# Kernel optimization log

Measured on AMD Instinct MI355X. Metric: run time of the kernel, lower is better.

Reference implementation:

```python
import jax, jax.numpy as jnp
import numpy as np

NUM_HEADS = 12
SAMPLING_RATIO = 0.5


def setup_inputs() -> dict:
    key = jax.random.key(0)
    k1, k2, k3, k4 = jax.random.split(key, 4)
    B, N, C = 4, 2048, 768
    x = jax.random.normal(k1, (B, N, C), dtype=jnp.float32)
    # nn.Linear(dim, 3*dim, bias=False): weight [3C, C]; we store transposed [C, 3C]
    w_qkv = jax.random.normal(k2, (C, 3 * C), dtype=jnp.float32) * (1.0 / np.sqrt(C))
    w_proj = jax.random.normal(k3, (C, C), dtype=jnp.float32) * (1.0 / np.sqrt(C))
    b_proj = jax.random.normal(k4, (C,), dtype=jnp.float32) * 0.01
    return {"x": x, "w_qkv": w_qkv, "w_proj": w_proj, "b_proj": b_proj}


def reference(x, w_qkv, w_proj, b_proj):
    B, N, C = x.shape
    H = NUM_HEADS
    hd = C // H
    scale = hd ** (-0.5)
    keep_num = int(N * SAMPLING_RATIO)

    qkv = (x @ w_qkv).reshape(B, N, 3, H, hd).transpose(2, 0, 3, 1, 4)  # [3,B,H,N,hd]
    q, k, v = qkv[0], qkv[1], qkv[2]

    # query-norm based token selection per (B, H)
    scores = jnp.linalg.norm(q, axis=-1)                     # [B,H,N]
    _, keep_idx = jax.lax.top_k(scores, keep_num)            # [B,H,keep]
    idx = keep_idx[..., None]                                # [B,H,keep,1]
    k_sel = jnp.take_along_axis(k, idx, axis=2)              # [B,H,keep,hd]
    v_sel = jnp.take_along_axis(v, idx, axis=2)              # [B,H,keep,hd]

    attn = jnp.einsum("bhnd,bhkd->bhnk", q, k_sel) * scale   # [B,H,N,keep]
    attn = jax.nn.softmax(jnp.clip(attn, -50.0, 50.0), axis=-1)
    out = jnp.einsum("bhnk,bhkd->bhnd", attn, v_sel)         # [B,H,N,hd]
    out = out.transpose(0, 2, 1, 3).reshape(B, N, C)
    return jnp.clip(out @ w_proj + b_proj, -10.0, 10.0)
```

## Files before the change

kernel.cpp:

```cpp
#include <hip/hip_runtime.h>
#include <hip/hip_bf16.h>
#include <math.h>


#define B_  4
#define N_  2048
#define C_  768
#define H_  12
#define HD_ 64
#define KEEP_ 1024
#define BH_ (B_ * H_)
#define GK  768

typedef __attribute__((ext_vector_type(8))) short short8v;
typedef __attribute__((ext_vector_type(4))) float f32x4;
typedef __attribute__((ext_vector_type(8))) _Float16 f16x8;
typedef __attribute__((ext_vector_type(4))) _Float16 f16x4;

__device__ inline unsigned short f2bf(float f) {
    unsigned u = __float_as_uint(f);
    unsigned r = (u + 0x7fffu + ((u >> 16) & 1u)) >> 16;
    return (unsigned short)r;
}
__device__ inline float bf2f(unsigned short h) {
    return __uint_as_float(((unsigned)h) << 16);
}

__device__ inline void gload16(const void* g, void* l) {
    __builtin_amdgcn_global_load_lds(
        (const __attribute__((address_space(1))) unsigned int*)(g),
        (__attribute__((address_space(3))) unsigned int*)(l), 16, 0, 0);
}

__global__ __launch_bounds__(256) void split4_kernel(
    const float* __restrict__ in, _Float16* __restrict__ hi,
    _Float16* __restrict__ lo, int n4)
{
    int i = blockIdx.x * 256 + threadIdx.x;
    if (i >= n4) return;
    float4 v = reinterpret_cast<const float4*>(in)[i];
    f16x4 h, l;
    h[0] = (_Float16)v.x; l[0] = (_Float16)(v.x - (float)h[0]);
    h[1] = (_Float16)v.y; l[1] = (_Float16)(v.y - (float)h[1]);
    h[2] = (_Float16)v.z; l[2] = (_Float16)(v.z - (float)h[2]);
    h[3] = (_Float16)v.w; l[3] = (_Float16)(v.w - (float)h[3]);
    reinterpret_cast<f16x4*>(hi)[i] = h;
    reinterpret_cast<f16x4*>(lo)[i] = l;
}

__global__ __launch_bounds__(256) void tsplit_kernel(
    const float* __restrict__ W, _Float16* __restrict__ Th,
    _Float16* __restrict__ Tl, int N)
{
    __shared__ float t[32][33];
    int n0 = blockIdx.x * 32, k0 = blockIdx.y * 32;
    int r = threadIdx.x >> 3, c4 = (threadIdx.x & 7) << 2;
    float4 v = *reinterpret_cast<const float4*>(&W[(size_t)(k0 + r) * N + n0 + c4]);
    t[r][c4 + 0] = v.x; t[r][c4 + 1] = v.y; t[r][c4 + 2] = v.z; t[r][c4 + 3] = v.w;
    __syncthreads();
#pragma unroll
    for (int j = 0; j < 4; ++j) {
        float val = t[c4 + j][r];
        _Float16 h = (_Float16)val;
        size_t o = (size_t)(n0 + r) * GK + k0 + c4 + j;
        Th[o] = h;
        Tl[o] = (_Float16)(val - (float)h);
    }
}

template <bool EPI>
__global__ __launch_bounds__(256, 2) void mfma_gemm(
    const _Float16* __restrict__ Ah, const _Float16* __restrict__ Al,
    const _Float16* __restrict__ Bh, const _Float16* __restrict__ Bl,
    float* __restrict__ C, int N, const float* __restrict__ bias,
    int gx, int cpx)
{
    __shared__ _Float16 lds[4][128 * 64];

    const int sb = ((int)blockIdx.x & 7) * cpx + ((int)blockIdx.x >> 3);
    const int bx = sb % gx, by = sb / gx;
    const int row0 = by * 128, col0 = bx * 128;

    const int tid = threadIdx.x;
    const int wave = tid >> 6, lane = tid & 63;
    const int fr = lane & 15, grp = lane >> 4;
    const int wr = wave >> 1, wc = wave & 1;

    const int dr = lane >> 3, ch = lane & 7;
    const int sc = (ch ^ dr) * 8;

    const _Float16* srcs[4] = {
        Ah + (size_t)row0 * GK, Al + (size_t)row0 * GK,
        Bh + (size_t)col0 * GK, Bl + (size_t)col0 * GK };

    f32x4 acc[4][4];
#pragma unroll
    for (int mt = 0; mt < 4; ++mt)
#pragma unroll
        for (int nt = 0; nt < 4; ++nt) acc[mt][nt] = (f32x4)0.f;

    const int swz0 = ((0 + grp) ^ (fr & 7)) * 16;
    const int swz1 = ((4 + grp) ^ (fr & 7)) * 16;

    for (int k0 = 0; k0 < GK; k0 += 64) {
        __syncthreads();
#pragma unroll
        for (int t = 0; t < 4; ++t) {
            const _Float16* gsrc = srcs[t] + k0 + sc;
#pragma unroll
            for (int i = 0; i < 4; ++i) {
                int rb = wave * 32 + i * 8;
                gload16(gsrc + (size_t)(rb + dr) * GK, &lds[t][rb * 64]);
            }
        }
        __syncthreads();

        f16x8 fa[4][2][2];
#pragma unroll
        for (int mt = 0; mt < 4; ++mt) {
            int rbyte = (wr * 64 + mt * 16 + fr) * 128;
            fa[mt][0][0] = *(const f16x8*)((const char*)lds[0] + rbyte + swz0);
            fa[mt][1][0] = *(const f16x8*)((const char*)lds[0] + rbyte + swz1);
            fa[mt][0][1] = *(const f16x8*)((const char*)lds[1] + rbyte + swz0);
            fa[mt][1][1] = *(const f16x8*)((const char*)lds[1] + rbyte + swz1);
        }
#pragma unroll
        for (int nt = 0; nt < 4; ++nt) {
            int rbyte = (wc * 64 + nt * 16 + fr) * 128;
            f16x8 bh0 = *(const f16x8*)((const char*)lds[2] + rbyte + swz0);
            f16x8 bh1 = *(const f16x8*)((const char*)lds[2] + rbyte + swz1);
            f16x8 bl0 = *(const f16x8*)((const char*)lds[3] + rbyte + swz0);
            f16x8 bl1 = *(const f16x8*)((const char*)lds[3] + rbyte + swz1);
#pragma unroll
            for (int mt = 0; mt < 4; ++mt) {
                acc[mt][nt] = __builtin_amdgcn_mfma_f32_16x16x32_f16(fa[mt][0][0], bh0, acc[mt][nt], 0, 0, 0);
                acc[mt][nt] = __builtin_amdgcn_mfma_f32_16x16x32_f16(fa[mt][0][0], bl0, acc[mt][nt], 0, 0, 0);
                acc[mt][nt] = __builtin_amdgcn_mfma_f32_16x16x32_f16(fa[mt][0][1], bh0, acc[mt][nt], 0, 0, 0);
                acc[mt][nt] = __builtin_amdgcn_mfma_f32_16x16x32_f16(fa[mt][1][0], bh1, acc[mt][nt], 0, 0, 0);
                acc[mt][nt] = __builtin_amdgcn_mfma_f32_16x16x32_f16(fa[mt][1][0], bl1, acc[mt][nt], 0, 0, 0);
                acc[mt][nt] = __builtin_amdgcn_mfma_f32_16x16x32_f16(fa[mt][1][1], bh1, acc[mt][nt], 0, 0, 0);
            }
        }
    }

#pragma unroll
    for (int mt = 0; mt < 4; ++mt)
#pragma unroll
        for (int nt = 0; nt < 4; ++nt) {
            int col = col0 + wc * 64 + nt * 16 + fr;
            float bv = 0.f;
            if (EPI) bv = bias[col];
#pragma unroll
            for (int r = 0; r < 4; ++r) {
                int row = row0 + wr * 64 + mt * 16 + grp * 4 + r;
                float v = acc[mt][nt][r];
                if (EPI) v = fminf(fmaxf(v + bv, -10.f), 10.f);
                C[(size_t)row * N + col] = v;
            }
        }
}

__global__ __launch_bounds__(256) void score_kernel(
    const float* __restrict__ qkv, float* __restrict__ scores,
    _Float16* __restrict__ q_h)
{
    int w = blockIdx.x * 4 + (threadIdx.x >> 6);
    int lane = threadIdx.x & 63;
    int bh = w >> 11;
    int n = w & (N_ - 1);
    int b = bh / H_, h = bh % H_;
    float q = qkv[((size_t)b * N_ + n) * (3 * C_) + (size_t)h * HD_ + lane];
    q_h[((size_t)bh * N_ + n) * HD_ + lane] = (_Float16)q;
    float ss = q * q;
#pragma unroll
    for (int off = 32; off; off >>= 1) ss += __shfl_xor(ss, off);
    if (lane == 0) scores[(size_t)bh * N_ + n] = ss;
}

__global__ __launch_bounds__(1024) void topk_kernel(
    const float* __restrict__ scores, int* __restrict__ keepidx)
{
    __shared__ unsigned long long keys[N_];
    const int bh = blockIdx.x;
    const int tid = threadIdx.x;
    const float* sc = scores + (size_t)bh * N_;
    for (int i = tid; i < N_; i += 1024) {
        unsigned fb = __float_as_uint(sc[i]);
        keys[i] = ((unsigned long long)fb << 32) | (unsigned)(N_ - 1 - i);
    }
    __syncthreads();
    for (int k = 2; k <= N_; k <<= 1) {
        for (int j = k >> 1; j > 0; j >>= 1) {
            for (int i = tid; i < N_; i += 1024) {
                int ixj = i ^ j;
                if (ixj > i) {
                    unsigned long long a = keys[i], b = keys[ixj];
                    bool desc = ((i & k) == 0);
                    if (desc ? (a < b) : (a > b)) { keys[i] = b; keys[ixj] = a; }
                }
            }
            __syncthreads();
        }
    }
    if (tid < KEEP_) {
        keepidx[(size_t)bh * KEEP_ + tid] = (N_ - 1) - (int)(keys[tid] & 0xffffffffu);
    }
}

__global__ __launch_bounds__(256) void gather_kernel(
    const float* __restrict__ qkv, const int* __restrict__ keepidx,
    _Float16* __restrict__ k_h, _Float16* __restrict__ k_l,
    unsigned short* __restrict__ vT_h, unsigned short* __restrict__ vT_l)
{
    __shared__ float vS[64][65];
    const int bh = blockIdx.x >> 4;
    const int chunk = blockIdx.x & 15;
    const int b = bh / H_, h = bh % H_;
    const int wave = threadIdx.x >> 6, lane = threadIdx.x & 63;
    const int j0 = chunk * 64;

#pragma unroll
    for (int jj = 0; jj < 16; ++jj) {
        int j = wave * 16 + jj;
        int n = keepidx[(size_t)bh * KEEP_ + j0 + j];
        size_t base = ((size_t)b * N_ + n) * (3 * C_) + (size_t)h * HD_ + lane;
        float kv = qkv[base + C_];
        float vv = qkv[base + 2 * C_];
        _Float16 kh = (_Float16)kv;
        size_t ko = ((size_t)bh * KEEP_ + j0 + j) * HD_ + lane;
        k_h[ko] = kh;
        k_l[ko] = (_Float16)(kv - (float)kh);
        vS[j][lane] = vv;
    }
    __syncthreads();
#pragma unroll
    for (int dd = 0; dd < 16; ++dd) {
        int d = wave * 16 + dd;
        float vv = vS[lane][d];
        unsigned short vh = f2bf(vv);
        size_t vo = ((size_t)bh * HD_ + d) * KEEP_ + j0 + lane;
        vT_h[vo] = vh;
        vT_l[vo] = f2bf(vv - bf2f(vh));
    }
}

__global__ __launch_bounds__(256, 2) void attn_kernel(
    const _Float16* __restrict__ q_h,
    const _Float16* __restrict__ k_h, const _Float16* __restrict__ k_l,
    const unsigned short* __restrict__ vT_h, const unsigned short* __restrict__ vT_l,
    _Float16* __restrict__ aoh, _Float16* __restrict__ aol)
{
    int bid = ((int)blockIdx.x & 7) * 96 + ((int)blockIdx.x >> 3);
    const int bh = bid >> 4;
    const int qt = bid & 15;
    const int b = bh / H_, h = bh - b * H_;
    const int wave = threadIdx.x >> 6;
    const int lane = threadIdx.x & 63;
    const int row16 = lane & 15;
    const int grp = lane >> 4;

    __shared__ unsigned short sKV[4][64 * 64];
    __shared__ unsigned short pH[4][32][72];

    const int n0 = qt * 128 + wave * 32;

    f16x8 aQ[2][2];
#pragma unroll
    for (int mt = 0; mt < 2; ++mt)
#pragma unroll
        for (int ks = 0; ks < 2; ++ks)
            aQ[mt][ks] = *reinterpret_cast<const f16x8*>(
                q_h + ((size_t)bh * N_ + n0 + mt * 16 + row16) * HD_ + ks * 32 + grp * 8);

    const int dr = lane >> 3, ch = lane & 7;
    const int sc8 = (ch ^ dr) * 8;
    const unsigned short* gbase;
    int rs, ts;
    if (wave == 0)      { gbase = (const unsigned short*)k_h + (size_t)bh * KEEP_ * HD_; rs = 64;   ts = 64 * HD_; }
    else if (wave == 1) { gbase = (const unsigned short*)k_l + (size_t)bh * KEEP_ * HD_; rs = 64;   ts = 64 * HD_; }
    else if (wave == 2) { gbase = vT_h + (size_t)bh * HD_ * KEEP_;                        rs = KEEP_; ts = 64; }
    else                { gbase = vT_l + (size_t)bh * HD_ * KEEP_;                        rs = KEEP_; ts = 64; }
    unsigned short* ldst = sKV[wave];

    f32x4 o[2][4];
    float ps[2][4];
#pragma unroll
    for (int mt = 0; mt < 2; ++mt)
#pragma unroll
        for (int nt = 0; nt < 4; ++nt) o[mt][nt] = (f32x4)0.f;
#pragma unroll
    for (int mt = 0; mt < 2; ++mt)
#pragma unroll
        for (int r = 0; r < 4; ++r) ps[mt][r] = 1e-30f;

    const int swzA = ((0 + grp) ^ (row16 & 7)) * 8;
    const int swzB = ((4 + grp) ^ (row16 & 7)) * 8;

    for (int t = 0; t < KEEP_ / 64; ++t) {
        __syncthreads();
#pragma unroll
        for (int i = 0; i < 8; ++i)
            gload16(gbase + (size_t)(i * 8 + dr) * rs + t * ts + sc8, ldst + i * 512);
        __syncthreads();

        f32x4 sv[2][4];
#pragma unroll
        for (int mt = 0; mt < 2; ++mt)
#pragma unroll
            for (int nt = 0; nt < 4; ++nt) sv[mt][nt] = (f32x4)0.f;
        const _Float16* sKh = (const _Float16*)sKV[0];
        const _Float16* sKl = (const _Float16*)sKV[1];
#pragma unroll
        for (int nt = 0; nt < 4; ++nt) {
            int rb = (nt * 16 + row16) * 64;
            f16x8 kh0 = *(const f16x8*)(sKh + rb + swzA);
            f16x8 kh1 = *(const f16x8*)(sKh + rb + swzB);
            f16x8 kl0 = *(const f16x8*)(sKl + rb + swzA);
            f16x8 kl1 = *(const f16x8*)(sKl + rb + swzB);
#pragma unroll
            for (int mt = 0; mt < 2; ++mt) {
                sv[mt][nt] = __builtin_amdgcn_mfma_f32_16x16x32_f16(aQ[mt][0], kh0, sv[mt][nt], 0, 0, 0);
                sv[mt][nt] = __builtin_amdgcn_mfma_f32_16x16x32_f16(aQ[mt][0], kl0, sv[mt][nt], 0, 0, 0);
                sv[mt][nt] = __builtin_amdgcn_mfma_f32_16x16x32_f16(aQ[mt][1], kh1, sv[mt][nt], 0, 0, 0);
                sv[mt][nt] = __builtin_amdgcn_mfma_f32_16x16x32_f16(aQ[mt][1], kl1, sv[mt][nt], 0, 0, 0);
            }
        }

#pragma unroll
        for (int mt = 0; mt < 2; ++mt)
#pragma unroll
            for (int nt = 0; nt < 4; ++nt)
#pragma unroll
                for (int r = 0; r < 4; ++r) {
                    float x = fminf(fmaxf(sv[mt][nt][r] * 0.125f, -50.f), 50.f);
                    float p = __expf(x - 50.f);
                    unsigned short ph = f2bf(p);
                    ps[mt][r] += bf2f(ph);
                    pH[wave][mt * 16 + grp * 4 + r][nt * 16 + row16] = ph;
                }

        short8v aP[2][2];
#pragma unroll
        for (int mt = 0; mt < 2; ++mt)
#pragma unroll
            for (int ks = 0; ks < 2; ++ks)
                aP[mt][ks] = *reinterpret_cast<const short8v*>(
                    &pH[wave][mt * 16 + row16][ks * 32 + grp * 8]);
        const unsigned short* sVh = sKV[2];
        const unsigned short* sVl = sKV[3];
#pragma unroll
        for (int nt = 0; nt < 4; ++nt) {
            int rb = (nt * 16 + row16) * 64;
            short8v vh0 = *(const short8v*)(sVh + rb + swzA);
            short8v vh1 = *(const short8v*)(sVh + rb + swzB);
            short8v vl0 = *(const short8v*)(sVl + rb + swzA);
            short8v vl1 = *(const short8v*)(sVl + rb + swzB);
#pragma unroll
            for (int mt = 0; mt < 2; ++mt) {
                o[mt][nt] = __builtin_amdgcn_mfma_f32_16x16x32_bf16(aP[mt][0], vh0, o[mt][nt], 0, 0, 0);
                o[mt][nt] = __builtin_amdgcn_mfma_f32_16x16x32_bf16(aP[mt][0], vl0, o[mt][nt], 0, 0, 0);
                o[mt][nt] = __builtin_amdgcn_mfma_f32_16x16x32_bf16(aP[mt][1], vh1, o[mt][nt], 0, 0, 0);
                o[mt][nt] = __builtin_amdgcn_mfma_f32_16x16x32_bf16(aP[mt][1], vl1, o[mt][nt], 0, 0, 0);
            }
        }
    }

#pragma unroll
    for (int off = 1; off < 16; off <<= 1)
#pragma unroll
        for (int mt = 0; mt < 2; ++mt)
#pragma unroll
            for (int r = 0; r < 4; ++r) ps[mt][r] += __shfl_xor(ps[mt][r], off);

#pragma unroll
    for (int mt = 0; mt < 2; ++mt)
#pragma unroll
        for (int nt = 0; nt < 4; ++nt)
#pragma unroll
            for (int r = 0; r < 4; ++r) {
                int n = n0 + mt * 16 + grp * 4 + r;
                int d = nt * 16 + row16;
                float v = o[mt][nt][r] / ps[mt][r];
                _Float16 hi = (_Float16)v;
                size_t oo = ((size_t)b * N_ + n) * C_ + (size_t)h * HD_ + d;
                aoh[oo] = hi;
                aol[oo] = (_Float16)(v - (float)hi);
            }
}

extern "C" void kernel_launch(void* const* d_in, const int* in_sizes, int n_in,
                              void* d_out, int out_size, void* d_ws, size_t ws_size,
                              hipStream_t stream)
{
    const float* x      = (const float*)d_in[0];
    const float* w_qkv  = (const float*)d_in[1];
    const float* w_proj = (const float*)d_in[2];
    const float* b_proj = (const float*)d_in[3];
    float* out = (float*)d_out;

    char* cur = (char*)d_ws;
    float* qkv = (float*)cur;              cur += (size_t)B_ * N_ * 3 * C_ * 4;
    float* scores = (float*)cur;           cur += (size_t)BH_ * N_ * 4;
    int* keepidx = (int*)cur;              cur += (size_t)BH_ * KEEP_ * 4;
    char* shared25 = cur;                  cur += (size_t)BH_ * N_ * HD_ * 2 * 2;
    _Float16* k_h = (_Float16*)cur;        cur += (size_t)BH_ * KEEP_ * HD_ * 2;
    _Float16* k_l = (_Float16*)cur;        cur += (size_t)BH_ * KEEP_ * HD_ * 2;
    unsigned short* vT_h = (unsigned short*)cur; cur += (size_t)BH_ * HD_ * KEEP_ * 2;
    unsigned short* vT_l = (unsigned short*)cur; cur += (size_t)BH_ * HD_ * KEEP_ * 2;
    _Float16* wTh = (_Float16*)cur;        cur += (size_t)(3 * C_) * GK * 2;
    _Float16* wTl = (_Float16*)cur;        cur += (size_t)(3 * C_) * GK * 2;

    _Float16* xh = (_Float16*)shared25;
    _Float16* xl = xh + (size_t)B_ * N_ * C_;
    _Float16* q_h = (_Float16*)shared25;
    _Float16* aoh = (_Float16*)qkv;
    _Float16* aol = aoh + (size_t)B_ * N_ * C_;

    const int n4x = (B_ * N_ * C_) / 4;

    split4_kernel<<<n4x / 256, 256, 0, stream>>>(x, xh, xl, n4x);
    tsplit_kernel<<<dim3((3 * C_) / 32, GK / 32), 256, 0, stream>>>(w_qkv, wTh, wTl, 3 * C_);
    mfma_gemm<false><<<(B_ * N_ / 128) * (3 * C_ / 128), 256, 0, stream>>>(
        xh, xl, wTh, wTl, qkv, 3 * C_, nullptr, (3 * C_) / 128, (B_ * N_ / 128) * (3 * C_ / 128) / 8);
    score_kernel<<<(BH_ * N_) / 4, 256, 0, stream>>>(qkv, scores, q_h);
    topk_kernel<<<BH_, 1024, 0, stream>>>(scores, keepidx);
    gather_kernel<<<BH_ * (KEEP_ / 64), 256, 0, stream>>>(qkv, keepidx, k_h, k_l, vT_h, vT_l);
    attn_kernel<<<BH_ * (N_ / 128), 256, 0, stream>>>(q_h, k_h, k_l, vT_h, vT_l, aoh, aol);
    tsplit_kernel<<<dim3(C_ / 32, GK / 32), 256, 0, stream>>>(w_proj, wTh, wTl, C_);
    mfma_gemm<true><<<(B_ * N_ / 128) * (C_ / 128), 256, 0, stream>>>(
        aoh, aol, wTh, wTl, out, C_, b_proj, C_ / 128, (B_ * N_ / 128) * (C_ / 128) / 8);
}
```

Measured before the change: 330.5 us.

## Fuse query-norm scoring into QKV GEMM and drop low-half A terms

The QKV GEMM epilogue for Q-column tiles now computes per-head squared norms and writes fp16 Q directly, which removes the separate score kernel and the fp32 Q write/read. K/V tiles skip the A low-half split, using 4 MFMAs instead of 6 per step, and store to a narrower KV buffer. The attention output is written only as a single fp16 value, and the projection GEMM uses the 4-MFMA path with no A-low term. These cuts cost some precision on K, V and the projection input.

```diff
diff --git a/kernel.cpp b/kernel.cpp
--- a/kernel.cpp
+++ b/kernel.cpp
@@ -11,6 +11,7 @@
 #define KEEP_ 1024
 #define BH_ (B_ * H_)
 #define GK  768
+#define KV2 1536
 
 typedef __attribute__((ext_vector_type(8))) short short8v;
 typedef __attribute__((ext_vector_type(4))) float f32x4;
@@ -68,11 +69,12 @@
     }
 }
 
-template <bool EPI>
+template <int MODE>
 __global__ __launch_bounds__(256, 2) void mfma_gemm(
     const _Float16* __restrict__ Ah, const _Float16* __restrict__ Al,
     const _Float16* __restrict__ Bh, const _Float16* __restrict__ Bl,
-    float* __restrict__ C, int N, const float* __restrict__ bias,
+    float* __restrict__ C, const float* __restrict__ bias,
+    float* __restrict__ scores, _Float16* __restrict__ q_h,
     int gx, int cpx)
 {
     __shared__ _Float16 lds[4][128 * 64];
@@ -80,6 +82,8 @@
     const int sb = ((int)blockIdx.x & 7) * cpx + ((int)blockIdx.x >> 3);
     const int bx = sb % gx, by = sb / gx;
     const int row0 = by * 128, col0 = bx * 128;
+
+    const bool qblk = (MODE == 0) && (bx < 6);
 
     const int tid = threadIdx.x;
     const int wave = tid >> 6, lane = tid & 63;
@@ -106,6 +110,7 @@
         __syncthreads();
 #pragma unroll
         for (int t = 0; t < 4; ++t) {
+            if (t == 1 && !qblk) continue;
             const _Float16* gsrc = srcs[t] + k0 + sc;
 #pragma unroll
             for (int i = 0; i < 4; ++i) {
@@ -115,66 +120,105 @@
         }
         __syncthreads();
 
-        f16x8 fa[4][2][2];
-#pragma unroll
-        for (int mt = 0; mt < 4; ++mt) {
-            int rbyte = (wr * 64 + mt * 16 + fr) * 128;
-            fa[mt][0][0] = *(const f16x8*)((const char*)lds[0] + rbyte + swz0);
-            fa[mt][1][0] = *(const f16x8*)((const char*)lds[0] + rbyte + swz1);
-            fa[mt][0][1] = *(const f16x8*)((const char*)lds[1] + rbyte + swz0);
-            fa[mt][1][1] = *(const f16x8*)((const char*)lds[1] + rbyte + swz1);
+        if (qblk) {
+            f16x8 fa[4][2][2];
+#pragma unroll
+            for (int mt = 0; mt < 4; ++mt) {
+                int rbyte = (wr * 64 + mt * 16 + fr) * 128;
+                fa[mt][0][0] = *(const f16x8*)((const char*)lds[0] + rbyte + swz0);
+                fa[mt][1][0] = *(const f16x8*)((const char*)lds[0] + rbyte + swz1);
+                fa[mt][0][1] = *(const f16x8*)((const char*)lds[1] + rbyte + swz0);
+                fa[mt][1][1] = *(const f16x8*)((const char*)lds[1] + rbyte + swz1);
+            }
+#pragma unroll
+            for (int nt = 0; nt < 4; ++nt) {
+                int rbyte = (wc * 64 + nt * 16 + fr) * 128;
+                f16x8 bh0 = *(const f16x8*)((const char*)lds[2] + rbyte + swz0);
+                f16x8 bh1 = *(const f16x8*)((const char*)lds[2] + rbyte + swz1);
+                f16x8 bl0 = *(const f16x8*)((const char*)lds[3] + rbyte + swz0);
+                f16x8 bl1 = *(const f16x8*)((const char*)lds[3] + rbyte + swz1);
+#pragma unroll
+                for (int mt = 0; mt < 4; ++mt) {
+                    acc[mt][nt] = __builtin_amdgcn_mfma_f32_16x16x32_f16(fa[mt][0][0], bh0, acc[mt][nt], 0, 0, 0);
+                    acc[mt][nt] = __builtin_amdgcn_mfma_f32_16x16x32_f16(fa[mt][0][0], bl0, acc[mt][nt], 0, 0, 0);
+                    acc[mt][nt] = __builtin_amdgcn_mfma_f32_16x16x32_f16(fa[mt][0][1], bh0, acc[mt][nt], 0, 0, 0);
+                    acc[mt][nt] = __builtin_amdgcn_mfma_f32_16x16x32_f16(fa[mt][1][0], bh1, acc[mt][nt], 0, 0, 0);
+                    acc[mt][nt] = __builtin_amdgcn_mfma_f32_16x16x32_f16(fa[mt][1][0], bl1, acc[mt][nt], 0, 0, 0);
+                    acc[mt][nt] = __builtin_amdgcn_mfma_f32_16x16x32_f16(fa[mt][1][1], bh1, acc[mt][nt], 0, 0, 0);
+                }
+            }
+        } else {
+            f16x8 fa[4][2];
+#pragma unroll
+            for (int mt = 0; mt < 4; ++mt) {
+                int rbyte = (wr * 64 + mt * 16 + fr) * 128;
+                fa[mt][0] = *(const f16x8*)((const char*)lds[0] + rbyte + swz0);
+                fa[mt][1] = *(const f16x8*)((const char*)lds[0] + rbyte + swz1);
+            }
+#pragma unroll
+            for (int nt = 0; nt < 4; ++nt) {
+                int rbyte = (wc * 64 + nt * 16 + fr) * 128;
+                f16x8 bh0 = *(const f16x8*)((const char*)lds[2] + rbyte + swz0);
+                f16x8 bh1 = *(const f16x8*)((const char*)lds[2] + rbyte + swz1);
+                f16x8 bl0 = *(const f16x8*)((const char*)lds[3] + rbyte + swz0);
+                f16x8 bl1 = *(const f16x8*)((const char*)lds[3] + rbyte + swz1);
+#pragma unroll
+                for (int mt = 0; mt < 4; ++mt) {
+                    acc[mt][nt] = __builtin_amdgcn_mfma_f32_16x16x32_f16(fa[mt][0], bh0, acc[mt][nt], 0, 0, 0);
+                    acc[mt][nt] = __builtin_amdgcn_mfma_f32_16x16x32_f16(fa[mt][0], bl0, acc[mt][nt], 0, 0, 0);
+                    acc[mt][nt] = __builtin_amdgcn_mfma_f32_16x16x32_f16(fa[mt][1], bh1, acc[mt][nt], 0, 0, 0);
+                    acc[mt][nt] = __builtin_amdgcn_mfma_f32_16x16x32_f16(fa[mt][1], bl1, acc[mt][nt], 0, 0, 0);
+                }
+            }
         }
-#pragma unroll
-        for (int nt = 0; nt < 4; ++nt) {
-            int rbyte = (wc * 64 + nt * 16 + fr) * 128;
-            f16x8 bh0 = *(const f16x8*)((const char*)lds[2] + rbyte + swz0);
-            f16x8 bh1 = *(const f16x8*)((const char*)lds[2] + rbyte + swz1);
-            f16x8 bl0 = *(const f16x8*)((const char*)lds[3] + rbyte + swz0);
-            f16x8 bl1 = *(const f16x8*)((const char*)lds[3] + rbyte + swz1);
-#pragma unroll
-            for (int mt = 0; mt < 4; ++mt) {
-                acc[mt][nt] = __builtin_amdgcn_mfma_f32_16x16x32_f16(fa[mt][0][0], bh0, acc[mt][nt], 0, 0, 0);
-                acc[mt][nt] = __builtin_amdgcn_mfma_f32_16x16x32_f16(fa[mt][0][0], bl0, acc[mt][nt], 0, 0, 0);
-                acc[mt][nt] = __builtin_amdgcn_mfma_f32_16x16x32_f16(fa[mt][0][1], bh0, acc[mt][nt], 0, 0, 0);
-                acc[mt][nt] = __builtin_amdgcn_mfma_f32_16x16x32_f16(fa[mt][1][0], bh1, acc[mt][nt], 0, 0, 0);
-                acc[mt][nt] = __builtin_amdgcn_mfma_f32_16x16x32_f16(fa[mt][1][0], bl1, acc[mt][nt], 0, 0, 0);
-                acc[mt][nt] = __builtin_amdgcn_mfma_f32_16x16x32_f16(fa[mt][1][1], bh1, acc[mt][nt], 0, 0, 0);
-            }
-        }
-    }
-
-#pragma unroll
-    for (int mt = 0; mt < 4; ++mt)
-#pragma unroll
-        for (int nt = 0; nt < 4; ++nt) {
-            int col = col0 + wc * 64 + nt * 16 + fr;
-            float bv = 0.f;
-            if (EPI) bv = bias[col];
+    }
+
+    if (MODE == 1) {
+#pragma unroll
+        for (int mt = 0; mt < 4; ++mt)
+#pragma unroll
+            for (int nt = 0; nt < 4; ++nt) {
+                int col = col0 + wc * 64 + nt * 16 + fr;
+                float bv = bias[col];
+#pragma unroll
+                for (int r = 0; r < 4; ++r) {
+                    int row = row0 + wr * 64 + mt * 16 + grp * 4 + r;
+                    float v = fminf(fmaxf(acc[mt][nt][r] + bv, -10.f), 10.f);
+                    C[(size_t)row * C_ + col] = v;
+                }
+            }
+    } else if (!qblk) {
+#pragma unroll
+        for (int mt = 0; mt < 4; ++mt)
+#pragma unroll
+            for (int nt = 0; nt < 4; ++nt) {
+                int col = col0 + wc * 64 + nt * 16 + fr - 768;
+#pragma unroll
+                for (int r = 0; r < 4; ++r) {
+                    int row = row0 + wr * 64 + mt * 16 + grp * 4 + r;
+                    C[(size_t)row * KV2 + col] = acc[mt][nt][r];
+                }
+            }
+    } else {
+        const int hglob = (col0 >> 6) + wc;
+#pragma unroll
+        for (int mt = 0; mt < 4; ++mt)
 #pragma unroll
             for (int r = 0; r < 4; ++r) {
+                float ss = 0.f;
+#pragma unroll
+                for (int nt = 0; nt < 4; ++nt) ss += acc[mt][nt][r] * acc[mt][nt][r];
+#pragma unroll
+                for (int off = 1; off < 16; off <<= 1) ss += __shfl_xor(ss, off);
                 int row = row0 + wr * 64 + mt * 16 + grp * 4 + r;
-                float v = acc[mt][nt][r];
-                if (EPI) v = fminf(fmaxf(v + bv, -10.f), 10.f);
-                C[(size_t)row * N + col] = v;
-            }
-        }
-}
-
-__global__ __launch_bounds__(256) void score_kernel(
-    const float* __restrict__ qkv, float* __restrict__ scores,
-    _Float16* __restrict__ q_h)
-{
-    int w = blockIdx.x * 4 + (threadIdx.x >> 6);
-    int lane = threadIdx.x & 63;
-    int bh = w >> 11;
-    int n = w & (N_ - 1);
-    int b = bh / H_, h = bh % H_;
-    float q = qkv[((size_t)b * N_ + n) * (3 * C_) + (size_t)h * HD_ + lane];
-    q_h[((size_t)bh * N_ + n) * HD_ + lane] = (_Float16)q;
-    float ss = q * q;
-#pragma unroll
-    for (int off = 32; off; off >>= 1) ss += __shfl_xor(ss, off);
-    if (lane == 0) scores[(size_t)bh * N_ + n] = ss;
+                int bb = row >> 11, n = row & (N_ - 1);
+                size_t bhn = ((size_t)bb * H_ + hglob) * N_ + n;
+                if (fr == 0) scores[bhn] = ss;
+#pragma unroll
+                for (int nt = 0; nt < 4; ++nt)
+                    q_h[bhn * HD_ + nt * 16 + fr] = (_Float16)acc[mt][nt][r];
+            }
+    }
 }
 
 __global__ __launch_bounds__(1024) void topk_kernel(
@@ -208,7 +252,7 @@
 }
 
 __global__ __launch_bounds__(256) void gather_kernel(
-    const float* __restrict__ qkv, const int* __restrict__ keepidx,
+    const float* __restrict__ kv, const int* __restrict__ keepidx,
     _Float16* __restrict__ k_h, _Float16* __restrict__ k_l,
     unsigned short* __restrict__ vT_h, unsigned short* __restrict__ vT_l)
 {
@@ -223,13 +267,13 @@
     for (int jj = 0; jj < 16; ++jj) {
         int j = wave * 16 + jj;
         int n = keepidx[(size_t)bh * KEEP_ + j0 + j];
-        size_t base = ((size_t)b * N_ + n) * (3 * C_) + (size_t)h * HD_ + lane;
-        float kv = qkv[base + C_];
-        float vv = qkv[base + 2 * C_];
-        _Float16 kh = (_Float16)kv;
+        size_t base = ((size_t)b * N_ + n) * KV2 + (size_t)h * HD_ + lane;
+        float kval = kv[base];
+        float vv = kv[base + C_];
+        _Float16 kh = (_Float16)kval;
         size_t ko = ((size_t)bh * KEEP_ + j0 + j) * HD_ + lane;
         k_h[ko] = kh;
-        k_l[ko] = (_Float16)(kv - (float)kh);
+        k_l[ko] = (_Float16)(kval - (float)kh);
         vS[j][lane] = vv;
     }
     __syncthreads();
@@ -248,7 +292,7 @@
     const _Float16* __restrict__ q_h,
     const _Float16* __restrict__ k_h, const _Float16* __restrict__ k_l,
     const unsigned short* __restrict__ vT_h, const unsigned short* __restrict__ vT_l,
-    _Float16* __restrict__ aoh, _Float16* __restrict__ aol)
+    _Float16* __restrict__ aoh)
 {
     int bid = ((int)blockIdx.x & 7) * 96 + ((int)blockIdx.x >> 3);
     const int bh = bid >> 4;
@@ -381,10 +425,7 @@
                 int n = n0 + mt * 16 + grp * 4 + r;
                 int d = nt * 16 + row16;
                 float v = o[mt][nt][r] / ps[mt][r];
-                _Float16 hi = (_Float16)v;
-                size_t oo = ((size_t)b * N_ + n) * C_ + (size_t)h * HD_ + d;
-                aoh[oo] = hi;
-                aol[oo] = (_Float16)(v - (float)hi);
+                aoh[((size_t)b * N_ + n) * C_ + (size_t)h * HD_ + d] = (_Float16)v;
             }
 }
 
@@ -399,10 +440,12 @@
     float* out = (float*)d_out;
 
     char* cur = (char*)d_ws;
-    float* qkv = (float*)cur;              cur += (size_t)B_ * N_ * 3 * C_ * 4;
+    float* kv = (float*)cur;               cur += (size_t)B_ * N_ * KV2 * 4;
     float* scores = (float*)cur;           cur += (size_t)BH_ * N_ * 4;
     int* keepidx = (int*)cur;              cur += (size_t)BH_ * KEEP_ * 4;
-    char* shared25 = cur;                  cur += (size_t)BH_ * N_ * HD_ * 2 * 2;
+    _Float16* xh = (_Float16*)cur;         cur += (size_t)B_ * N_ * C_ * 2;
+    _Float16* xl = (_Float16*)cur;         cur += (size_t)B_ * N_ * C_ * 2;
+    _Float16* q_h = (_Float16*)cur;        cur += (size_t)BH_ * N_ * HD_ * 2;
     _Float16* k_h = (_Float16*)cur;        cur += (size_t)BH_ * KEEP_ * HD_ * 2;
     _Float16* k_l = (_Float16*)cur;        cur += (size_t)BH_ * KEEP_ * HD_ * 2;
     unsigned short* vT_h = (unsigned short*)cur; cur += (size_t)BH_ * HD_ * KEEP_ * 2;
@@ -410,23 +453,20 @@
     _Float16* wTh = (_Float16*)cur;        cur += (size_t)(3 * C_) * GK * 2;
     _Float16* wTl = (_Float16*)cur;        cur += (size_t)(3 * C_) * GK * 2;
 
-    _Float16* xh = (_Float16*)shared25;
-    _Float16* xl = xh + (size_t)B_ * N_ * C_;
-    _Float16* q_h = (_Float16*)shared25;
-    _Float16* aoh = (_Float16*)qkv;
-    _Float16* aol = aoh + (size_t)B_ * N_ * C_;
+    _Float16* aoh = xh;
 
     const int n4x = (B_ * N_ * C_) / 4;
 
     split4_kernel<<<n4x / 256, 256, 0, stream>>>(x, xh, xl, n4x);
     tsplit_kernel<<<dim3((3 * C_) / 32, GK / 32), 256, 0, stream>>>(w_qkv, wTh, wTl, 3 * C_);
-    mfma_gemm<false><<<(B_ * N_ / 128) * (3 * C_ / 128), 256, 0, stream>>>(
-        xh, xl, wTh, wTl, qkv, 3 * C_, nullptr, (3 * C_) / 128, (B_ * N_ / 128) * (3 * C_ / 128) / 8);
-    score_kernel<<<(BH_ * N_) / 4, 256, 0, stream>>>(qkv, scores, q_h);
+    mfma_gemm<0><<<(B_ * N_ / 128) * (3 * C_ / 128), 256, 0, stream>>>(
+        xh, xl, wTh, wTl, kv, nullptr, scores, q_h,
+        (3 * C_) / 128, (B_ * N_ / 128) * (3 * C_ / 128) / 8);
     topk_kernel<<<BH_, 1024, 0, stream>>>(scores, keepidx);
-    gather_kernel<<<BH_ * (KEEP_ / 64), 256, 0, stream>>>(qkv, keepidx, k_h, k_l, vT_h, vT_l);
-    attn_kernel<<<BH_ * (N_ / 128), 256, 0, stream>>>(q_h, k_h, k_l, vT_h, vT_l, aoh, aol);
+    gather_kernel<<<BH_ * (KEEP_ / 64), 256, 0, stream>>>(kv, keepidx, k_h, k_l, vT_h, vT_l);
+    attn_kernel<<<BH_ * (N_ / 128), 256, 0, stream>>>(q_h, k_h, k_l, vT_h, vT_l, aoh);
     tsplit_kernel<<<dim3(C_ / 32, GK / 32), 256, 0, stream>>>(w_proj, wTh, wTl, C_);
-    mfma_gemm<true><<<(B_ * N_ / 128) * (C_ / 128), 256, 0, stream>>>(
-        aoh, aol, wTh, wTl, out, C_, b_proj, C_ / 128, (B_ * N_ / 128) * (C_ / 128) / 8);
-}
+    mfma_gemm<1><<<(B_ * N_ / 128) * (C_ / 128), 256, 0, stream>>>(
+        aoh, aoh, wTh, wTl, out, b_proj, nullptr, nullptr,
+        C_ / 128, (B_ * N_ / 128) * (C_ / 128) / 8);
+}
```

Result: faster. 305.8 us (-7.5%).
